# Kernel tuning notes

Hardware: AMD Instinct MI355X
Metric: run time of the kernel (lower is better)

The kernel has to match this reference:

```python
import jax, jax.numpy as jnp
import numpy as np

BN_EPS = 1e-5


def _guide_net(fullres, w1, b1, bn_gamma, bn_beta, bn_mean, bn_var, w2, b2):
    # two 1x1 convs == channel matmuls
    x = jnp.einsum('nchw,oc->nohw', fullres, w1[:, :, 0, 0]) + b1[None, :, None, None]
    inv = bn_gamma / jnp.sqrt(bn_var + BN_EPS)
    x = (x - bn_mean[None, :, None, None]) * inv[None, :, None, None] + bn_beta[None, :, None, None]
    x = jax.nn.relu(x)
    g = jnp.einsum('nchw,oc->nohw', x, w2[:, :, 0, 0]) + b2[None, :, None, None]
    return jax.nn.sigmoid(g)  # [N,1,H,W] in (0,1)


def _slice_one(grid_n, guide_n):
    # grid_n: [C,D,h,w]; guide_n: [H,W]; trilinear grid_sample, align_corners=True.
    C, D, h, w = grid_n.shape
    H, W = guide_n.shape
    # normalized coords in torch code map exactly to voxel coords [0, size-1]
    gz = guide_n * (D - 1)                      # per-pixel depth coord [H,W]
    z0f = jnp.floor(gz)
    tz = (gz - z0f)[None, :, :]                 # [1,H,W]
    z0 = jnp.clip(z0f, 0, D - 1).astype(jnp.int32)
    z1 = jnp.clip(z0f + 1, 0, D - 1).astype(jnp.int32)
    gy = jnp.linspace(0.0, h - 1.0, H)
    y0f = jnp.floor(gy)
    ty = (gy - y0f)[None, :, None]              # [1,H,1]
    y0 = jnp.clip(y0f, 0, h - 1).astype(jnp.int32)[:, None]
    y1 = jnp.clip(y0f + 1, 0, h - 1).astype(jnp.int32)[:, None]
    gx = jnp.linspace(0.0, w - 1.0, W)
    x0f = jnp.floor(gx)
    tx = (gx - x0f)[None, None, :]              # [1,1,W]
    x0 = jnp.clip(x0f, 0, w - 1).astype(jnp.int32)[None, :]
    x1 = jnp.clip(x0f + 1, 0, w - 1).astype(jnp.int32)[None, :]

    def g(z, y, x):
        # z:[H,W], y:[H,1], x:[1,W] -> broadcast gather -> [C,H,W]
        return grid_n[:, z, y, x]

    def lerp_xy(z):
        a = g(z, y0, x0) * (1 - tx) + g(z, y0, x1) * tx
        b = g(z, y1, x0) * (1 - tx) + g(z, y1, x1) * tx
        return a * (1 - ty) + b * ty

    return lerp_xy(z0) * (1 - tz) + lerp_xy(z1) * tz  # [C,H,W]


def _apply_coeffs(coeff, fullres):
    # coeff: [N,12,H,W]; rows (0:3,+3), (4:7,+7), (8:11,+11)
    N, _, H, W = coeff.shape
    A = coeff[:, jnp.array([0, 1, 2, 4, 5, 6, 8, 9, 10])].reshape(N, 3, 3, H, W)
    bias = coeff[:, jnp.array([3, 7, 11])]
    return jnp.einsum('nkchw,nchw->nkhw', A, fullres) + bias


def setup_inputs() -> dict:
    key = jax.random.key(0)
    ks = jax.random.split(key, 10)
    N, H, W = 2, 1080, 1920
    return {
        'fullres': jax.random.uniform(ks[0], (N, 3, H, W), jnp.float32),
        'bilateral_grid': jax.random.normal(ks[1], (N, 12, 8, 16, 16), jnp.float32),
        'w1': jax.random.normal(ks[2], (16, 3, 1, 1), jnp.float32) * 0.2,
        'b1': jax.random.normal(ks[3], (16,), jnp.float32) * 0.1,
        'bn_gamma': jax.random.uniform(ks[4], (16,), jnp.float32, 0.5, 1.5),
        'bn_beta': jax.random.normal(ks[5], (16,), jnp.float32) * 0.1,
        'bn_mean': jax.random.normal(ks[6], (16,), jnp.float32) * 0.1,
        'bn_var': jax.random.uniform(ks[7], (16,), jnp.float32, 0.5, 1.5),
        'w2': jax.random.normal(ks[8], (1, 16, 1, 1), jnp.float32) * 0.2,
        'b2': jax.random.normal(ks[9], (1,), jnp.float32) * 0.1,
    }


def reference(fullres, bilateral_grid, w1, b1, bn_gamma, bn_beta, bn_mean, bn_var, w2, b2):
    guide = _guide_net(fullres, w1, b1, bn_gamma, bn_beta, bn_mean, bn_var, w2, b2)  # [N,1,H,W]
    coeff = jax.vmap(_slice_one)(bilateral_grid, guide[:, 0])                         # [N,12,H,W]
    return _apply_coeffs(coeff, fullres)                                              # [N,3,H,W]
```

## Files before the change

kernel.cpp:

```cpp
#include <hip/hip_runtime.h>
#include <hip/hip_bf16.h>
#include <math.h>

#define HWV (1080 * 1920)

typedef _Float16 half2 __attribute__((ext_vector_type(2)));
typedef __fp16   pk2   __attribute__((ext_vector_type(2)));
union U32H2 { unsigned u; half2 h; pk2 p; };

__global__ void prep_w(const float* __restrict__ w1, const float* __restrict__ b1,
                       const float* __restrict__ gamma, const float* __restrict__ beta,
                       const float* __restrict__ mean, const float* __restrict__ var,
                       const float* __restrict__ w2, const float* __restrict__ b2,
                       float* __restrict__ wsw) {
    int i = blockIdx.x * blockDim.x + threadIdx.x;
    unsigned* wp = (unsigned*)(wsw + 84);
    if (i < 16) {
        float inv = gamma[i] / sqrtf(var[i] + 1e-5f);
        float wr = w1[i*3+0] * inv, wg = w1[i*3+1] * inv, wb = w1[i*3+2] * inv;
        float bs = (b1[i] - mean[i]) * inv + beta[i];
        U32H2 t;
        t.p = __builtin_amdgcn_cvt_pkrtz(wr, wr); wp[i*4+0] = t.u;
        t.p = __builtin_amdgcn_cvt_pkrtz(wg, wg); wp[i*4+1] = t.u;
        t.p = __builtin_amdgcn_cvt_pkrtz(wb, wb); wp[i*4+2] = t.u;
        t.p = __builtin_amdgcn_cvt_pkrtz(bs, bs); wp[i*4+3] = t.u;
        float w2c = w2[i];
        t.p = __builtin_amdgcn_cvt_pkrtz(w2c, w2c); wp[64 + i] = t.u;
    }
    if (i == 16) {
        float b2s = b2[0];
        U32H2 t;
        t.p = __builtin_amdgcn_cvt_pkrtz(b2s, b2s); wp[80] = t.u;
    }
    if (i < 1920) {
        float gx = (float)i * (15.0f / 1919.0f);
        float x0f = floorf(gx);
        float tx = gx - x0f;
        int x0 = (int)x0f;
        int x1 = min(x0 + 1, 15);
        U32H2 a0, a1;
        a0.p = __builtin_amdgcn_cvt_pkrtz(1.0f - tx, 1.0f - tx);
        a1.p = __builtin_amdgcn_cvt_pkrtz(tx, tx);
        uint4* colinfo = (uint4*)(wsw + 168);
        colinfo[i] = make_uint4((unsigned)(x0 | (x1 << 8)), a0.u, a1.u, 0u);
    }
}

__global__ __launch_bounds__(512, 8) void fused_kernel(
        const float* __restrict__ fullres,
        const float* __restrict__ grid,
        const float* __restrict__ wsw,
        float* __restrict__ out) {
    __shared__ unsigned slo[9][9][4];
    __shared__ unsigned shi[9][9][2];

    const int tid = threadIdx.x;
    const int seg = blockIdx.x;
    const int n   = blockIdx.y;
    const int y   = blockIdx.z;
    const int xs  = seg * 1024;
    const int x   = xs + 2 * tid;
    const bool act = (x < 1920);
    const int a = (int)((float)xs * (15.0f / 1919.0f));
    const int pcol = min(x, 1918);
    const int p = y * 1920 + pcol;

    const float* fr = fullres + n * 3 * HWV + p;
    float2 R = *(const float2*)(fr);
    float2 G = *(const float2*)(fr + HWV);
    float2 B = *(const float2*)(fr + 2 * HWV);
    const uint4* colinfo = (const uint4*)(wsw + 168);
    uint4 ci0 = colinfo[pcol];
    uint4 ci1 = colinfo[pcol + 1];

    if (tid < 486) {
        float gy = (float)y * (15.0f / 1079.0f);
        float y0f = floorf(gy);
        float ty = gy - y0f;
        int y0 = min((int)y0f, 15);
        int y1 = min(y0 + 1, 15);
        const int dy = (y1 - y0) * 16;
        int j   = tid / 81;
        int rem = tid - j * 81;
        int z   = rem / 9;
        int k   = rem - z * 9;
        int zz  = min(z, 7);
        int xc  = min(a + k, 15);
        const float* q0 = grid + n * 24576 + (2 * j) * 2048 + zz * 256 + y0 * 16 + xc;
        const float* q1 = q0 + 2048;
        float v00 = q0[0], v01 = q0[dy];
        float v10 = q1[0], v11 = q1[dy];
        float e0 = fmaf(ty, v01 - v00, v00);
        float e1 = fmaf(ty, v11 - v10, v10);
        U32H2 t;
        t.p = __builtin_amdgcn_cvt_pkrtz(e0, e1);
        if (j < 4) slo[k][z][j] = t.u;
        else       shi[k][z][j - 4] = t.u;
    }
    __syncthreads();

    if (!act) return;

    U32H2 rr, gg, bb;
    rr.p = __builtin_amdgcn_cvt_pkrtz(R.x, R.y);
    gg.p = __builtin_amdgcn_cvt_pkrtz(G.x, G.y);
    bb.p = __builtin_amdgcn_cvt_pkrtz(B.x, B.y);
    const unsigned* wp = (const unsigned*)(wsw + 84);
    const half2 zero = {(_Float16)0.0f, (_Float16)0.0f};
    U32H2 accp; accp.u = wp[80];
#pragma unroll
    for (int c = 0; c < 16; ++c) {
        U32H2 wr, wg, wb, bs, w2d;
        wr.u = wp[4*c+0]; wg.u = wp[4*c+1]; wb.u = wp[4*c+2]; bs.u = wp[4*c+3];
        w2d.u = wp[64 + c];
        half2 h = wr.h * rr.h + (wg.h * gg.h + (wb.h * bb.h + bs.h));
        h = __builtin_elementwise_max(h, zero);
        accp.h = h * w2d.h + accp.h;
    }
    float accv[2] = {(float)accp.h.x, (float)accp.h.y};

    float rv[2] = {R.x, R.y}, gv[2] = {G.x, G.y}, bv[2] = {B.x, B.y};
    float outr[2], outg[2], outb[2];
    uint4 civ[2] = {ci0, ci1};

#pragma unroll
    for (int q = 0; q < 2; ++q) {
        float e = __expf(-accv[q]);
        float guide = __builtin_amdgcn_rcpf(1.0f + e);
        float gz = guide * 7.0f;
        float z0f = floorf(gz);
        float tz = gz - z0f;
        int z0 = min((int)z0f, 7);
        int z1 = z0 + 1;

        int k0 = (int)(civ[q].x & 255u) - a;
        int k1 = (int)((civ[q].x >> 8) & 255u) - a;
        U32H2 wx0d, wx1d;
        wx0d.u = civ[q].y;
        wx1d.u = civ[q].z;

        U32H2 wz0d, wz1d;
        wz0d.p = __builtin_amdgcn_cvt_pkrtz(1.0f - tz, 1.0f - tz);
        wz1d.p = __builtin_amdgcn_cvt_pkrtz(tz, tz);

        half2 w00 = wx0d.h * wz0d.h;
        half2 w01 = wx0d.h * wz1d.h;
        half2 w10 = wx1d.h * wz0d.h;
        half2 w11 = wx1d.h * wz1d.h;

        const uint4 A0 = *(const uint4*)&slo[k0][z0][0];
        const uint4 A1 = *(const uint4*)&slo[k0][z1][0];
        const uint4 B0 = *(const uint4*)&slo[k1][z0][0];
        const uint4 B1 = *(const uint4*)&slo[k1][z1][0];
        const uint2 C0 = *(const uint2*)&shi[k0][z0][0];
        const uint2 C1 = *(const uint2*)&shi[k0][z1][0];
        const uint2 D0 = *(const uint2*)&shi[k1][z0][0];
        const uint2 D1 = *(const uint2*)&shi[k1][z1][0];

        unsigned a0j[6] = {A0.x, A0.y, A0.z, A0.w, C0.x, C0.y};
        unsigned a1j[6] = {A1.x, A1.y, A1.z, A1.w, C1.x, C1.y};
        unsigned b0j[6] = {B0.x, B0.y, B0.z, B0.w, D0.x, D0.y};
        unsigned b1j[6] = {B1.x, B1.y, B1.z, B1.w, D1.x, D1.y};

        half2 hc[6];
#pragma unroll
        for (int j = 0; j < 6; ++j) {
            U32H2 ua0, ua1, ub0, ub1;
            ua0.u = a0j[j]; ua1.u = a1j[j]; ub0.u = b0j[j]; ub1.u = b1j[j];
            half2 h = w00 * ua0.h + (w01 * ua1.h);
            h = w10 * ub0.h + h;
            h = w11 * ub1.h + h;
            hc[j] = h;
        }

        outr[q] = fmaf((float)hc[0].x, rv[q], fmaf((float)hc[0].y, gv[q],
                  fmaf((float)hc[1].x, bv[q], (float)hc[1].y)));
        outg[q] = fmaf((float)hc[2].x, rv[q], fmaf((float)hc[2].y, gv[q],
                  fmaf((float)hc[3].x, bv[q], (float)hc[3].y)));
        outb[q] = fmaf((float)hc[4].x, rv[q], fmaf((float)hc[4].y, gv[q],
                  fmaf((float)hc[5].x, bv[q], (float)hc[5].y)));
    }

    float* op = out + n * 3 * HWV + p;
    *(float2*)(op)           = make_float2(outr[0], outr[1]);
    *(float2*)(op + HWV)     = make_float2(outg[0], outg[1]);
    *(float2*)(op + 2 * HWV) = make_float2(outb[0], outb[1]);
}

extern "C" void kernel_launch(void* const* d_in, const int* in_sizes, int n_in,
                              void* d_out, int out_size, void* d_ws, size_t ws_size,
                              hipStream_t stream) {
    const float* fullres = (const float*)d_in[0];
    const float* grid    = (const float*)d_in[1];
    const float* w1      = (const float*)d_in[2];
    const float* b1      = (const float*)d_in[3];
    const float* gamma   = (const float*)d_in[4];
    const float* beta    = (const float*)d_in[5];
    const float* mean    = (const float*)d_in[6];
    const float* var     = (const float*)d_in[7];
    const float* w2      = (const float*)d_in[8];
    const float* b2      = (const float*)d_in[9];
    float* out = (float*)d_out;

    float* wsw = (float*)d_ws;

    prep_w<<<8, 256, 0, stream>>>(w1, b1, gamma, beta, mean, var, w2, b2, wsw);

    dim3 grid_dim(2, 2, 1080);
    fused_kernel<<<grid_dim, 512, 0, stream>>>(fullres, grid, wsw, out);
}
```

Baseline: 31.00 us.

## Split guide computation into separate kernel with quantized guide buffer

Moves the guide network (two 1x1 convs, ReLU, sigmoid) out of the fused slicing kernel into its own kernel. That kernel processes four pixels per thread and writes the guide as a 16-bit fixed-point value (3 bits of z index, 12 bits of fraction). The slice kernel then reads this value instead of recomputing the guide, which shortens its per-thread ALU work. In exchange the fullres tensor is read twice and an extra guide buffer is written and read, which adds memory traffic to a bandwidth-bound workload. It also adds a fallback to the old fused kernel when the workspace is too small.

```diff
diff --git a/kernel.cpp b/kernel.cpp
--- a/kernel.cpp
+++ b/kernel.cpp
@@ -3,6 +3,7 @@
 #include <math.h>
 
 #define HWV (1080 * 1920)
+#define NPIX (2 * HWV)
 
 typedef _Float16 half2 __attribute__((ext_vector_type(2)));
 typedef __fp16   pk2   __attribute__((ext_vector_type(2)));
@@ -46,10 +47,60 @@
     }
 }
 
-__global__ __launch_bounds__(512, 8) void fused_kernel(
+__global__ __launch_bounds__(256) void guide_kernel(
+        const float* __restrict__ fullres,
+        const float* __restrict__ wsw,
+        unsigned short* __restrict__ gp) {
+    int i = blockIdx.x * 256 + threadIdx.x;
+    int n  = i / (HWV / 4);
+    int pi = (i - n * (HWV / 4)) * 4;
+    const float* fr = fullres + n * 3 * HWV + pi;
+    float4 R = *(const float4*)(fr);
+    float4 G = *(const float4*)(fr + HWV);
+    float4 B = *(const float4*)(fr + 2 * HWV);
+
+    U32H2 r01, r23, g01, g23, b01, b23;
+    r01.p = __builtin_amdgcn_cvt_pkrtz(R.x, R.y);
+    r23.p = __builtin_amdgcn_cvt_pkrtz(R.z, R.w);
+    g01.p = __builtin_amdgcn_cvt_pkrtz(G.x, G.y);
+    g23.p = __builtin_amdgcn_cvt_pkrtz(G.z, G.w);
+    b01.p = __builtin_amdgcn_cvt_pkrtz(B.x, B.y);
+    b23.p = __builtin_amdgcn_cvt_pkrtz(B.z, B.w);
+    const unsigned* wp = (const unsigned*)(wsw + 84);
+    const half2 zero = {(_Float16)0.0f, (_Float16)0.0f};
+    U32H2 acc01, acc23;
+    acc01.u = wp[80];
+    acc23.u = wp[80];
+#pragma unroll
+    for (int c = 0; c < 16; ++c) {
+        U32H2 wr, wg, wb, bs, w2d;
+        wr.u = wp[4*c+0]; wg.u = wp[4*c+1]; wb.u = wp[4*c+2]; bs.u = wp[4*c+3];
+        w2d.u = wp[64 + c];
+        half2 h01 = wr.h * r01.h + (wg.h * g01.h + (wb.h * b01.h + bs.h));
+        half2 h23 = wr.h * r23.h + (wg.h * g23.h + (wb.h * b23.h + bs.h));
+        h01 = __builtin_elementwise_max(h01, zero);
+        h23 = __builtin_elementwise_max(h23, zero);
+        acc01.h = h01 * w2d.h + acc01.h;
+        acc23.h = h23 * w2d.h + acc23.h;
+    }
+    float accv[4] = {(float)acc01.h.x, (float)acc01.h.y,
+                     (float)acc23.h.x, (float)acc23.h.y};
+    unsigned short us[4];
+#pragma unroll
+    for (int q = 0; q < 4; ++q) {
+        float e = __expf(-accv[q]);
+        float guide = __builtin_amdgcn_rcpf(1.0f + e);
+        us[q] = (unsigned short)(guide * 28672.0f);
+    }
+    ushort4 o = make_ushort4(us[0], us[1], us[2], us[3]);
+    *(ushort4*)(gp + n * HWV + pi) = o;
+}
+
+__global__ __launch_bounds__(512, 8) void slice_kernel(
         const float* __restrict__ fullres,
         const float* __restrict__ grid,
         const float* __restrict__ wsw,
+        const unsigned short* __restrict__ gp,
         float* __restrict__ out) {
     __shared__ unsigned slo[9][9][4];
     __shared__ unsigned shi[9][9][2];
@@ -69,6 +120,7 @@
     float2 R = *(const float2*)(fr);
     float2 G = *(const float2*)(fr + HWV);
     float2 B = *(const float2*)(fr + 2 * HWV);
+    unsigned gpu = *(const unsigned*)(gp + n * HWV + p);
     const uint4* colinfo = (const uint4*)(wsw + 168);
     uint4 ci0 = colinfo[pcol];
     uint4 ci1 = colinfo[pcol + 1];
@@ -101,6 +153,126 @@
 
     if (!act) return;
 
+    float rv[2] = {R.x, R.y}, gv[2] = {G.x, G.y}, bv[2] = {B.x, B.y};
+    float outr[2], outg[2], outb[2];
+    uint4 civ[2] = {ci0, ci1};
+
+#pragma unroll
+    for (int q = 0; q < 2; ++q) {
+        unsigned u = (q == 0) ? (gpu & 0xFFFFu) : (gpu >> 16);
+        int z0 = (int)(u >> 12);
+        int z1 = z0 + 1;
+        float tz = (float)(u & 4095u) * (1.0f / 4096.0f);
+
+        int k0 = (int)(civ[q].x & 255u) - a;
+        int k1 = (int)((civ[q].x >> 8) & 255u) - a;
+        U32H2 wx0d, wx1d;
+        wx0d.u = civ[q].y;
+        wx1d.u = civ[q].z;
+
+        U32H2 wz0d, wz1d;
+        wz0d.p = __builtin_amdgcn_cvt_pkrtz(1.0f - tz, 1.0f - tz);
+        wz1d.p = __builtin_amdgcn_cvt_pkrtz(tz, tz);
+
+        half2 w00 = wx0d.h * wz0d.h;
+        half2 w01 = wx0d.h * wz1d.h;
+        half2 w10 = wx1d.h * wz0d.h;
+        half2 w11 = wx1d.h * wz1d.h;
+
+        const uint4 A0 = *(const uint4*)&slo[k0][z0][0];
+        const uint4 A1 = *(const uint4*)&slo[k0][z1][0];
+        const uint4 B0 = *(const uint4*)&slo[k1][z0][0];
+        const uint4 B1 = *(const uint4*)&slo[k1][z1][0];
+        const uint2 C0 = *(const uint2*)&shi[k0][z0][0];
+        const uint2 C1 = *(const uint2*)&shi[k0][z1][0];
+        const uint2 D0 = *(const uint2*)&shi[k1][z0][0];
+        const uint2 D1 = *(const uint2*)&shi[k1][z1][0];
+
+        unsigned a0j[6] = {A0.x, A0.y, A0.z, A0.w, C0.x, C0.y};
+        unsigned a1j[6] = {A1.x, A1.y, A1.z, A1.w, C1.x, C1.y};
+        unsigned b0j[6] = {B0.x, B0.y, B0.z, B0.w, D0.x, D0.y};
+        unsigned b1j[6] = {B1.x, B1.y, B1.z, B1.w, D1.x, D1.y};
+
+        half2 hc[6];
+#pragma unroll
+        for (int j = 0; j < 6; ++j) {
+            U32H2 ua0, ua1, ub0, ub1;
+            ua0.u = a0j[j]; ua1.u = a1j[j]; ub0.u = b0j[j]; ub1.u = b1j[j];
+            half2 h = w00 * ua0.h + (w01 * ua1.h);
+            h = w10 * ub0.h + h;
+            h = w11 * ub1.h + h;
+            hc[j] = h;
+        }
+
+        outr[q] = fmaf((float)hc[0].x, rv[q], fmaf((float)hc[0].y, gv[q],
+                  fmaf((float)hc[1].x, bv[q], (float)hc[1].y)));
+        outg[q] = fmaf((float)hc[2].x, rv[q], fmaf((float)hc[2].y, gv[q],
+                  fmaf((float)hc[3].x, bv[q], (float)hc[3].y)));
+        outb[q] = fmaf((float)hc[4].x, rv[q], fmaf((float)hc[4].y, gv[q],
+                  fmaf((float)hc[5].x, bv[q], (float)hc[5].y)));
+    }
+
+    float* op = out + n * 3 * HWV + p;
+    *(float2*)(op)           = make_float2(outr[0], outr[1]);
+    *(float2*)(op + HWV)     = make_float2(outg[0], outg[1]);
+    *(float2*)(op + 2 * HWV) = make_float2(outb[0], outb[1]);
+}
+
+__global__ __launch_bounds__(512, 8) void fused_kernel(
+        const float* __restrict__ fullres,
+        const float* __restrict__ grid,
+        const float* __restrict__ wsw,
+        float* __restrict__ out) {
+    __shared__ unsigned slo[9][9][4];
+    __shared__ unsigned shi[9][9][2];
+
+    const int tid = threadIdx.x;
+    const int seg = blockIdx.x;
+    const int n   = blockIdx.y;
+    const int y   = blockIdx.z;
+    const int xs  = seg * 1024;
+    const int x   = xs + 2 * tid;
+    const bool act = (x < 1920);
+    const int a = (int)((float)xs * (15.0f / 1919.0f));
+    const int pcol = min(x, 1918);
+    const int p = y * 1920 + pcol;
+
+    const float* fr = fullres + n * 3 * HWV + p;
+    float2 R = *(const float2*)(fr);
+    float2 G = *(const float2*)(fr + HWV);
+    float2 B = *(const float2*)(fr + 2 * HWV);
+    const uint4* colinfo = (const uint4*)(wsw + 168);
+    uint4 ci0 = colinfo[pcol];
+    uint4 ci1 = colinfo[pcol + 1];
+
+    if (tid < 486) {
+        float gy = (float)y * (15.0f / 1079.0f);
+        float y0f = floorf(gy);
+        float ty = gy - y0f;
+        int y0 = min((int)y0f, 15);
+        int y1 = min(y0 + 1, 15);
+        const int dy = (y1 - y0) * 16;
+        int j   = tid / 81;
+        int rem = tid - j * 81;
+        int z   = rem / 9;
+        int k   = rem - z * 9;
+        int zz  = min(z, 7);
+        int xc  = min(a + k, 15);
+        const float* q0 = grid + n * 24576 + (2 * j) * 2048 + zz * 256 + y0 * 16 + xc;
+        const float* q1 = q0 + 2048;
+        float v00 = q0[0], v01 = q0[dy];
+        float v10 = q1[0], v11 = q1[dy];
+        float e0 = fmaf(ty, v01 - v00, v00);
+        float e1 = fmaf(ty, v11 - v10, v10);
+        U32H2 t;
+        t.p = __builtin_amdgcn_cvt_pkrtz(e0, e1);
+        if (j < 4) slo[k][z][j] = t.u;
+        else       shi[k][z][j - 4] = t.u;
+    }
+    __syncthreads();
+
+    if (!act) return;
+
     U32H2 rr, gg, bb;
     rr.p = __builtin_amdgcn_cvt_pkrtz(R.x, R.y);
     gg.p = __builtin_amdgcn_cvt_pkrtz(G.x, G.y);
@@ -206,6 +378,16 @@
 
     prep_w<<<8, 256, 0, stream>>>(w1, b1, gamma, beta, mean, var, w2, b2, wsw);
 
-    dim3 grid_dim(2, 2, 1080);
-    fused_kernel<<<grid_dim, 512, 0, stream>>>(fullres, grid, wsw, out);
-}
+    const size_t GP_OFF = 65536;
+    const size_t need   = GP_OFF + (size_t)NPIX * 2;
+
+    if (ws_size >= need) {
+        unsigned short* gp = (unsigned short*)((char*)d_ws + GP_OFF);
+        guide_kernel<<<NPIX / 4 / 256, 256, 0, stream>>>(fullres, wsw, gp);
+        dim3 grid_dim(2, 2, 1080);
+        slice_kernel<<<grid_dim, 512, 0, stream>>>(fullres, grid, wsw, gp, out);
+    } else {
+        dim3 grid_dim(2, 2, 1080);
+        fused_kernel<<<grid_dim, 512, 0, stream>>>(fullres, grid, wsw, out);
+    }
+}
```

Measured after the change: 42.88 us. 1.38x slower.
